# Kernel optimization log

Measured on AMD Instinct MI355X. Metric: run time of the kernel, lower is better.

## Reference

```python
import jax, jax.numpy as jnp
import numpy as np

DIM = 128
HEADS = 4
WIN = 7
N = WIN * WIN  # 49 tokens per window
B = 64         # images
BDIM = 64      # windows per image (56/7)^2
B_ = B * BDIM  # 4096 total windows
HEAD_DIM = DIM // HEADS
SCALE = HEAD_DIM ** (-0.5)


def _rel_index():
    ch, cw = np.meshgrid(np.arange(WIN), np.arange(WIN), indexing='ij')
    coords = np.stack([ch.ravel(), cw.ravel()])            # [2, N]
    rel = coords[:, :, None] - coords[:, None, :]          # [2, N, N]
    rel = rel.transpose(1, 2, 0).astype(np.int32)
    rel[:, :, 0] += WIN - 1
    rel[:, :, 1] += WIN - 1
    rel[:, :, 0] *= 2 * WIN - 1
    return jnp.asarray(rel.sum(-1))                        # [N, N] in [0, 169)


def setup_inputs() -> dict:
    key = jax.random.key(0)
    ks = jax.random.split(key, 7)
    return {
        'x': jax.random.normal(ks[0], (B_, N, DIM), jnp.float32),
        'q_global': jax.random.normal(ks[1], (B, 1, HEADS, N, HEAD_DIM), jnp.float32),
        'rel_bias_table': jax.random.normal(ks[2], (169, HEADS), jnp.float32) * 0.02,
        'W_kv': jax.random.normal(ks[3], (DIM, 2 * DIM), jnp.float32) / np.sqrt(DIM),
        'b_kv': jnp.zeros((2 * DIM,), jnp.float32),
        'W_proj': jax.random.normal(ks[4], (DIM, DIM), jnp.float32) / np.sqrt(DIM),
        'b_proj': jnp.zeros((DIM,), jnp.float32),
        'rel_index': _rel_index(),
    }


def reference(x, q_global, rel_bias_table, W_kv, b_kv, W_proj, b_proj, rel_index):
    Bw, n, C = x.shape
    Bg = q_global.shape[0]
    bdim = Bw // Bg
    # kv projection: [B_, N, 2, H, hd] -> k, v each [B_, H, N, hd]
    kv = (x @ W_kv + b_kv).reshape(Bw, n, 2, HEADS, HEAD_DIM)
    kv = kv.transpose(2, 0, 3, 1, 4)
    k, v = kv[0], kv[1]
    # broadcast global q over windows of each image
    q = jnp.broadcast_to(q_global, (Bg, bdim, HEADS, n, HEAD_DIM)).reshape(Bw, HEADS, n, HEAD_DIM)
    attn = jnp.einsum('bhnd,bhmd->bhnm', q * SCALE, k)
    bias = rel_bias_table[rel_index]                        # [N, N, H]
    attn = attn + bias.transpose(2, 0, 1)[None]
    attn = jax.nn.softmax(attn, axis=-1)
    out = jnp.einsum('bhnm,bhmd->bhnd', attn, v)
    out = out.transpose(0, 2, 1, 3).reshape(Bw, n, C)
    return out @ W_proj + b_proj
```

## Files before the change

### kernel.cpp

```cpp
#include <hip/hip_runtime.h>

#define SCALE 0.17677669529663687f

typedef __attribute__((ext_vector_type(8))) short bf16x8;
typedef __attribute__((ext_vector_type(4))) float f32x4;

__device__ inline short cvt_bf16(float f) {
    union { float f; unsigned u; } v; v.f = f;
    unsigned r = v.u + 0x7fffu + ((v.u >> 16) & 1u);
    return (short)(r >> 16);
}
__device__ inline short cvt_bf16_fast(float f) {
    union { float f; unsigned u; } v; v.f = f;
    return (short)((v.u + 0x8000u) >> 16);
}
__device__ inline unsigned pack_bf16x2(float f0, float f1) {
    union { float f; unsigned u; } a, b; a.f = f0; b.f = f1;
    return __builtin_amdgcn_perm(b.u + 0x8000u, a.u + 0x8000u, 0x07060302u);
}

#define WS_WPT  32768
#define WS_QW   49152
#define WS_BIAS 450560

__global__ void prep_kernel(const float* __restrict__ qg,
                            const float* __restrict__ rbt,
                            const float* __restrict__ wkv,
                            const float* __restrict__ wpj,
                            const int*   __restrict__ ridx,
                            short* __restrict__ ws) {
    int i = blockIdx.x * 256 + threadIdx.x;
    if (i < 32768) {
        int c = i >> 7, k = i & 127;
        ws[i] = cvt_bf16(wkv[k * 256 + c]);
        return;
    }
    i -= 32768;
    if (i < 16384) {
        int c = i >> 7, k = i & 127;
        ws[WS_WPT + i] = cvt_bf16(wpj[k * 128 + c]);
        return;
    }
    i -= 16384;
    if (i < 100352) {
        float4 q4 = *(const float4*)(qg + (long)i * 4);
        unsigned lo = (unsigned)(unsigned short)cvt_bf16(q4.x * SCALE) |
                      ((unsigned)(unsigned short)cvt_bf16(q4.y * SCALE) << 16);
        unsigned hi = (unsigned)(unsigned short)cvt_bf16(q4.z * SCALE) |
                      ((unsigned)(unsigned short)cvt_bf16(q4.w * SCALE) << 16);
        uint2 u; u.x = lo; u.y = hi;
        *(uint2*)(ws + WS_QW + (long)i * 4) = u;
        return;
    }
    i -= 100352;
    if (i < 12544) {
        int h = i / 3136, rem = i % 3136, ir = rem >> 6, j = rem & 63;
        float* bias = (float*)(ws + WS_BIAS);
        bias[i] = (j < 49) ? rbt[ridx[ir * 49 + j] * 4 + h] : 0.f;
    }
}

#define PSLOT   3136
#define VOFF    12544
#define VSTR    56
#define SMEM_SZ 19776

__global__ __launch_bounds__(256, 4) void win_attn_kernel(
        const float* __restrict__ x,
        const short* __restrict__ ws,
        const float* __restrict__ bkv,
        const float* __restrict__ bpj,
        float* __restrict__ out) {
    const int b    = blockIdx.x;
    const int img  = b >> 6;
    const int tid  = threadIdx.x;
    const int w    = tid >> 6;
    const int lane = tid & 63;
    const int quad = lane >> 4;
    const int l16  = lane & 15;

    const short* wkvt  = ws;
    const short* wpt   = ws + WS_WPT;
    const short* qw    = ws + WS_QW;
    const float* biasb = (const float*)(ws + WS_BIAS);

    __shared__ __align__(16) short smem[SMEM_SZ];
    short* xs = smem;
    short* os = smem;

    if (tid < 64) smem[19712 + tid] = 0;

    const f32x4 fzero = {0.f, 0.f, 0.f, 0.f};
    const int h = w;

    const float* xb = x + (long)b * 49 * 128;
    #pragma unroll
    for (int it = 0; it < 4; ++it) {
        int chunk = tid + it * 256;
        if (chunk < 784) {
            int row = chunk >> 4, c8 = (chunk & 15) * 8;
            const float* p = xb + row * 128 + c8;
            float4 a = *(const float4*)p;
            float4 c = *(const float4*)(p + 4);
            union { uint4 u; bf16x8 v; } pk;
            pk.u.x = pack_bf16x2(a.x, a.y);
            pk.u.y = pack_bf16x2(a.z, a.w);
            pk.u.z = pack_bf16x2(c.x, c.y);
            pk.u.w = pack_bf16x2(c.z, c.w);
            *(bf16x8*)(xs + row * 136 + c8) = pk.v;
        }
    }
    __syncthreads();

    f32x4 acc[4][4];
    #pragma unroll
    for (int nt = 0; nt < 4; ++nt)
        #pragma unroll
        for (int mi = 0; mi < 4; ++mi) acc[nt][mi] = fzero;

    #pragma unroll
    for (int kk = 0; kk < 4; ++kk) {
        bf16x8 bfr[4];
        #pragma unroll
        for (int nt = 0; nt < 4; ++nt)
            bfr[nt] = *(const bf16x8*)(wkvt + ((w * 4 + nt) * 16 + l16) * 128 + kk * 32 + quad * 8);
        #pragma unroll
        for (int mi = 0; mi < 4; ++mi) {
            int tok = mi * 16 + l16; if (tok > 48) tok = 48;
            bf16x8 af = *(const bf16x8*)(xs + tok * 136 + kk * 32 + quad * 8);
            #pragma unroll
            for (int nt = 0; nt < 4; ++nt)
                acc[nt][mi] = __builtin_amdgcn_mfma_f32_16x16x32_bf16(af, bfr[nt], acc[nt][mi], 0, 0, 0);
        }
    }
    __syncthreads();

    #pragma unroll
    for (int nt = 0; nt < 4; ++nt) {
        const int c = (w * 4 + nt) * 16 + l16;
        const float bv = bkv[c];
        if (c < 128) {
            int hh = c >> 5, d = c & 31;
            short* kdst = smem + hh * PSLOT + d;
            #pragma unroll
            for (int mi = 0; mi < 4; ++mi)
                #pragma unroll
                for (int r = 0; r < 4; ++r) {
                    int tok = mi * 16 + quad * 4 + r;
                    kdst[tok * 40] = cvt_bf16_fast(acc[nt][mi][r] + bv);
                }
        } else {
            int cv = c - 128, hh = cv >> 5, d = cv & 31;
            short* vdst = smem + VOFF + (hh * 32 + d) * VSTR;
            #pragma unroll
            for (int mi = 0; mi < 4; ++mi) {
                int tok0 = mi * 16 + quad * 4;
                if (tok0 < VSTR) {
                    *(unsigned*)(vdst + tok0)     = pack_bf16x2(acc[nt][mi][0] + bv, acc[nt][mi][1] + bv);
                    *(unsigned*)(vdst + tok0 + 2) = pack_bf16x2(acc[nt][mi][2] + bv, acc[nt][mi][3] + bv);
                }
            }
        }
    }
    __syncthreads();

    short* ksh = smem + h * PSLOT;
    const short* qh = qw + (long)(img * 4 + h) * 49 * 32;
    bf16x8 qfrag[4];
    #pragma unroll
    for (int ni = 0; ni < 4; ++ni) {
        int i = ni * 16 + l16; if (i > 48) i = 48;
        qfrag[ni] = *(const bf16x8*)(qh + i * 32 + quad * 8);
    }
    bf16x8 kfrag[4];
    #pragma unroll
    for (int mi = 0; mi < 4; ++mi)
        kfrag[mi] = *(const bf16x8*)(ksh + (mi * 16 + l16) * 40 + quad * 8);

    #pragma unroll
    for (int ni = 0; ni < 4; ++ni) {
        f32x4 sacc[4] = {fzero, fzero, fzero, fzero};
        #pragma unroll
        for (int mi = 0; mi < 4; ++mi)
            sacc[mi] = __builtin_amdgcn_mfma_f32_16x16x32_bf16(kfrag[mi], qfrag[ni], sacc[mi], 0, 0, 0);

        int itok = ni * 16 + l16;
        int ic = itok > 48 ? 48 : itok;
        const float* bp = biasb + (h * 49 + ic) * 64;
        float v[16];
        #pragma unroll
        for (int mi = 0; mi < 4; ++mi) {
            float4 b4 = *(const float4*)(bp + mi * 16 + quad * 4);
            float bb[4] = {b4.x, b4.y, b4.z, b4.w};
            #pragma unroll
            for (int r = 0; r < 4; ++r) {
                int j = mi * 16 + quad * 4 + r;
                v[mi * 4 + r] = (j < 49) ? (sacc[mi][r] + bb[r]) : -3.0e38f;
            }
        }
        float m = v[0];
        #pragma unroll
        for (int t = 1; t < 16; ++t) m = fmaxf(m, v[t]);
        m = fmaxf(m, __shfl_xor(m, 16, 64));
        m = fmaxf(m, __shfl_xor(m, 32, 64));
        float sum = 0.f;
        #pragma unroll
        for (int t = 0; t < 16; ++t) { float e = __expf(v[t] - m); v[t] = e; sum += e; }
        sum += __shfl_xor(sum, 16, 64);
        sum += __shfl_xor(sum, 32, 64);
        float inv = 1.0f / sum;
        if (itok < 49) {
            #pragma unroll
            for (int mi = 0; mi < 4; ++mi) {
                int jo8 = mi * 2 + (quad >> 1);
                int off = itok * 64 + ((jo8 ^ (itok & 7)) << 3) + ((quad & 1) << 2);
                uint2 u;
                u.x = pack_bf16x2(v[mi * 4 + 0] * inv, v[mi * 4 + 1] * inv);
                u.y = pack_bf16x2(v[mi * 4 + 2] * inv, v[mi * 4 + 3] * inv);
                *(uint2*)(ksh + off) = u;
            }
        }
    }

    f32x4 oacc[4][2];
    #pragma unroll
    for (int mo = 0; mo < 4; ++mo)
        #pragma unroll
        for (int nt = 0; nt < 2; ++nt) oacc[mo][nt] = fzero;
    #pragma unroll
    for (int kk = 0; kk < 2; ++kk) {
        bf16x8 pfrag[4];
        #pragma unroll
        for (int mo = 0; mo < 4; ++mo) {
            int row = mo * 16 + l16; if (row > 48) row = 48;
            int jo8 = kk * 4 + quad;
            pfrag[mo] = *(const bf16x8*)(ksh + row * 64 + ((jo8 ^ (row & 7)) << 3));
        }
        #pragma unroll
        for (int nt = 0; nt < 2; ++nt) {
            bf16x8 vfrag = *(const bf16x8*)(smem + VOFF + (h * 32 + nt * 16 + l16) * VSTR + kk * 32 + quad * 8);
            #pragma unroll
            for (int mo = 0; mo < 4; ++mo)
                oacc[mo][nt] = __builtin_amdgcn_mfma_f32_16x16x32_bf16(pfrag[mo], vfrag, oacc[mo][nt], 0, 0, 0);
        }
    }
    __syncthreads();

    #pragma unroll
    for (int mo = 0; mo < 4; ++mo)
        #pragma unroll
        for (int nt = 0; nt < 2; ++nt)
            #pragma unroll
            for (int r = 0; r < 4; ++r) {
                int tok = mo * 16 + quad * 4 + r;
                os[tok * 136 + h * 32 + nt * 16 + l16] = cvt_bf16_fast(oacc[mo][nt][r]);
            }
    __syncthreads();

    f32x4 pacc[2][4];
    #pragma unroll
    for (int ct = 0; ct < 2; ++ct)
        #pragma unroll
        for (int mi = 0; mi < 4; ++mi) pacc[ct][mi] = fzero;
    #pragma unroll
    for (int kk = 0; kk < 4; ++kk) {
        bf16x8 ofrag[4];
        #pragma unroll
        for (int mi = 0; mi < 4; ++mi)
            ofrag[mi] = *(const bf16x8*)(os + (mi * 16 + l16) * 136 + kk * 32 + quad * 8);
        #pragma unroll
        for (int ct = 0; ct < 2; ++ct) {
            const int c0 = (w * 2 + ct) * 16;
            bf16x8 wfrag = *(const bf16x8*)(wpt + (c0 + l16) * 128 + kk * 32 + quad * 8);
            #pragma unroll
            for (int mi = 0; mi < 4; ++mi)
                pacc[ct][mi] = __builtin_amdgcn_mfma_f32_16x16x32_bf16(ofrag[mi], wfrag, pacc[ct][mi], 0, 0, 0);
        }
    }
    #pragma unroll
    for (int ct = 0; ct < 2; ++ct) {
        const int c0 = (w * 2 + ct) * 16;
        const float bb = bpj[c0 + l16];
        #pragma unroll
        for (int mi = 0; mi < 4; ++mi)
            #pragma unroll
            for (int r = 0; r < 4; ++r) {
                int tok = mi * 16 + quad * 4 + r;
                if (tok < 49)
                    out[((long)b * 49 + tok) * 128 + c0 + l16] = pacc[ct][mi][r] + bb;
            }
    }
}

extern "C" void kernel_launch(void* const* d_in, const int* in_sizes, int n_in,
                              void* d_out, int out_size, void* d_ws, size_t ws_size,
                              hipStream_t stream) {
    const float* x    = (const float*)d_in[0];
    const float* qg   = (const float*)d_in[1];
    const float* rbt  = (const float*)d_in[2];
    const float* wkv  = (const float*)d_in[3];
    const float* bkv  = (const float*)d_in[4];
    const float* wpj  = (const float*)d_in[5];
    const float* bpj  = (const float*)d_in[6];
    const int*   ridx = (const int*)d_in[7];
    short* ws = (short*)d_ws;

    const int prep_total = 32768 + 16384 + 100352 + 12544;
    prep_kernel<<<(prep_total + 255) / 256, 256, 0, stream>>>(qg, rbt, wkv, wpj, ridx, ws);
    win_attn_kernel<<<4096, 256, 0, stream>>>(x, ws, bkv, bpj, (float*)d_out);
}
```

Measured before the change: 251.8 us.

## Keep V and softmax probabilities in registers, feeding PV MFMA directly per head

Each wave now computes the K and V columns for its own head in the KV projection, so V stays in registers as 16x16x16 MFMA B fragments instead of going through shared memory. The softmax output is packed straight into A fragments for a 16x16x16 bf16 MFMA, removing the P round trip through LDS and two block barriers. LDS use shrinks, allowing launch bounds of 5 blocks per CU, at the cost of more live registers and a smaller-K MFMA instruction for the PV product.

```diff
diff --git a/kernel.cpp b/kernel.cpp
--- a/kernel.cpp
+++ b/kernel.cpp
@@ -3,6 +3,7 @@
 #define SCALE 0.17677669529663687f
 
 typedef __attribute__((ext_vector_type(8))) short bf16x8;
+typedef __attribute__((ext_vector_type(4))) short bf16x4;
 typedef __attribute__((ext_vector_type(4))) float f32x4;
 
 __device__ inline short cvt_bf16(float f) {
@@ -18,6 +19,17 @@
     union { float f; unsigned u; } a, b; a.f = f0; b.f = f1;
     return __builtin_amdgcn_perm(b.u + 0x8000u, a.u + 0x8000u, 0x07060302u);
 }
+
+#if __has_builtin(__builtin_amdgcn_mfma_f32_16x16x16bf16_1k)
+__device__ inline f32x4 mfma16x16(bf16x4 a, bf16x4 b, f32x4 c) {
+    return __builtin_amdgcn_mfma_f32_16x16x16bf16_1k(a, b, c, 0, 0, 0);
+}
+#else
+__device__ inline f32x4 mfma16x16(bf16x4 a, bf16x4 b, f32x4 c) {
+    asm("v_mfma_f32_16x16x16_bf16 %0, %1, %2, %0" : "+v"(c) : "v"(a), "v"(b));
+    return c;
+}
+#endif
 
 #define WS_WPT  32768
 #define WS_QW   49152
@@ -60,12 +72,11 @@
     }
 }
 
-#define PSLOT   3136
-#define VOFF    12544
-#define VSTR    56
-#define SMEM_SZ 19776
-
-__global__ __launch_bounds__(256, 4) void win_attn_kernel(
+#define KOFF    6664
+#define KSLOT   1960
+#define SMEM_SZ 14504
+
+__global__ __launch_bounds__(256, 5) void win_attn_kernel(
         const float* __restrict__ x,
         const short* __restrict__ ws,
         const float* __restrict__ bkv,
@@ -87,8 +98,6 @@
     __shared__ __align__(16) short smem[SMEM_SZ];
     short* xs = smem;
     short* os = smem;
-
-    if (tid < 64) smem[19712 + tid] = 0;
 
     const f32x4 fzero = {0.f, 0.f, 0.f, 0.f};
     const int h = w;
@@ -122,8 +131,10 @@
     for (int kk = 0; kk < 4; ++kk) {
         bf16x8 bfr[4];
         #pragma unroll
-        for (int nt = 0; nt < 4; ++nt)
-            bfr[nt] = *(const bf16x8*)(wkvt + ((w * 4 + nt) * 16 + l16) * 128 + kk * 32 + quad * 8);
+        for (int nt = 0; nt < 4; ++nt) {
+            int col = ((nt < 2) ? (h * 32 + nt * 16) : (128 + h * 32 + (nt - 2) * 16)) + l16;
+            bfr[nt] = *(const bf16x8*)(wkvt + col * 128 + kk * 32 + quad * 8);
+        }
         #pragma unroll
         for (int mi = 0; mi < 4; ++mi) {
             int tok = mi * 16 + l16; if (tok > 48) tok = 48;
@@ -133,61 +144,53 @@
                 acc[nt][mi] = __builtin_amdgcn_mfma_f32_16x16x32_bf16(af, bfr[nt], acc[nt][mi], 0, 0, 0);
         }
     }
-    __syncthreads();
-
-    #pragma unroll
-    for (int nt = 0; nt < 4; ++nt) {
-        const int c = (w * 4 + nt) * 16 + l16;
-        const float bv = bkv[c];
-        if (c < 128) {
-            int hh = c >> 5, d = c & 31;
-            short* kdst = smem + hh * PSLOT + d;
-            #pragma unroll
-            for (int mi = 0; mi < 4; ++mi)
-                #pragma unroll
-                for (int r = 0; r < 4; ++r) {
-                    int tok = mi * 16 + quad * 4 + r;
-                    kdst[tok * 40] = cvt_bf16_fast(acc[nt][mi][r] + bv);
-                }
-        } else {
-            int cv = c - 128, hh = cv >> 5, d = cv & 31;
-            short* vdst = smem + VOFF + (hh * 32 + d) * VSTR;
-            #pragma unroll
-            for (int mi = 0; mi < 4; ++mi) {
-                int tok0 = mi * 16 + quad * 4;
-                if (tok0 < VSTR) {
-                    *(unsigned*)(vdst + tok0)     = pack_bf16x2(acc[nt][mi][0] + bv, acc[nt][mi][1] + bv);
-                    *(unsigned*)(vdst + tok0 + 2) = pack_bf16x2(acc[nt][mi][2] + bv, acc[nt][mi][3] + bv);
-                }
-            }
-        }
-    }
-    __syncthreads();
-
-    short* ksh = smem + h * PSLOT;
+
+    short* ksl = smem + KOFF + h * KSLOT;
+    #pragma unroll
+    for (int nt = 0; nt < 2; ++nt) {
+        const int d = nt * 16 + l16;
+        const float bv = bkv[h * 32 + d];
+        short* kdst = ksl + d;
+        #pragma unroll
+        for (int mi = 0; mi < 4; ++mi)
+            #pragma unroll
+            for (int r = 0; r < 4; ++r) {
+                int tok = mi * 16 + quad * 4 + r;
+                if (tok < 49) kdst[tok * 40] = cvt_bf16_fast(acc[nt][mi][r] + bv);
+            }
+    }
+    bf16x4 vfrag[2][4];
+    #pragma unroll
+    for (int nv = 0; nv < 2; ++nv) {
+        const float bv = bkv[128 + h * 32 + nv * 16 + l16];
+        #pragma unroll
+        for (int kt = 0; kt < 4; ++kt) {
+            union { unsigned u[2]; bf16x4 v; } pk;
+            pk.u[0] = pack_bf16x2(acc[nv + 2][kt][0] + bv, acc[nv + 2][kt][1] + bv);
+            pk.u[1] = pack_bf16x2(acc[nv + 2][kt][2] + bv, acc[nv + 2][kt][3] + bv);
+            vfrag[nv][kt] = pk.v;
+        }
+    }
+
     const short* qh = qw + (long)(img * 4 + h) * 49 * 32;
-    bf16x8 qfrag[4];
+    f32x4 oacc[4][2];
+    #pragma unroll
+    for (int mo = 0; mo < 4; ++mo)
+        #pragma unroll
+        for (int nv = 0; nv < 2; ++nv) oacc[mo][nv] = fzero;
+
     #pragma unroll
     for (int ni = 0; ni < 4; ++ni) {
-        int i = ni * 16 + l16; if (i > 48) i = 48;
-        qfrag[ni] = *(const bf16x8*)(qh + i * 32 + quad * 8);
-    }
-    bf16x8 kfrag[4];
-    #pragma unroll
-    for (int mi = 0; mi < 4; ++mi)
-        kfrag[mi] = *(const bf16x8*)(ksh + (mi * 16 + l16) * 40 + quad * 8);
-
-    #pragma unroll
-    for (int ni = 0; ni < 4; ++ni) {
+        int ic = ni * 16 + l16; if (ic > 48) ic = 48;
+        bf16x8 qf = *(const bf16x8*)(qh + ic * 32 + quad * 8);
         f32x4 sacc[4] = {fzero, fzero, fzero, fzero};
         #pragma unroll
-        for (int mi = 0; mi < 4; ++mi)
-            sacc[mi] = __builtin_amdgcn_mfma_f32_16x16x32_bf16(kfrag[mi], qfrag[ni], sacc[mi], 0, 0, 0);
-
-        int itok = ni * 16 + l16;
-        int ic = itok > 48 ? 48 : itok;
+        for (int mi = 0; mi < 4; ++mi) {
+            int kr = mi * 16 + l16; if (kr > 48) kr = 48;
+            bf16x8 kf = *(const bf16x8*)(ksl + kr * 40 + quad * 8);
+            sacc[mi] = __builtin_amdgcn_mfma_f32_16x16x32_bf16(kf, qf, sacc[mi], 0, 0, 0);
+        }
         const float* bp = biasb + (h * 49 + ic) * 64;
-        float v[16];
         #pragma unroll
         for (int mi = 0; mi < 4; ++mi) {
             float4 b4 = *(const float4*)(bp + mi * 16 + quad * 4);
@@ -195,65 +198,48 @@
             #pragma unroll
             for (int r = 0; r < 4; ++r) {
                 int j = mi * 16 + quad * 4 + r;
-                v[mi * 4 + r] = (j < 49) ? (sacc[mi][r] + bb[r]) : -3.0e38f;
-            }
-        }
-        float m = v[0];
-        #pragma unroll
-        for (int t = 1; t < 16; ++t) m = fmaxf(m, v[t]);
+                sacc[mi][r] = (j < 49) ? (sacc[mi][r] + bb[r]) : -3.0e38f;
+            }
+        }
+        float m = -3.0e38f;
+        #pragma unroll
+        for (int mi = 0; mi < 4; ++mi)
+            #pragma unroll
+            for (int r = 0; r < 4; ++r) m = fmaxf(m, sacc[mi][r]);
         m = fmaxf(m, __shfl_xor(m, 16, 64));
         m = fmaxf(m, __shfl_xor(m, 32, 64));
         float sum = 0.f;
         #pragma unroll
-        for (int t = 0; t < 16; ++t) { float e = __expf(v[t] - m); v[t] = e; sum += e; }
+        for (int mi = 0; mi < 4; ++mi)
+            #pragma unroll
+            for (int r = 0; r < 4; ++r) {
+                float e = __expf(sacc[mi][r] - m);
+                sacc[mi][r] = e; sum += e;
+            }
         sum += __shfl_xor(sum, 16, 64);
         sum += __shfl_xor(sum, 32, 64);
         float inv = 1.0f / sum;
-        if (itok < 49) {
-            #pragma unroll
-            for (int mi = 0; mi < 4; ++mi) {
-                int jo8 = mi * 2 + (quad >> 1);
-                int off = itok * 64 + ((jo8 ^ (itok & 7)) << 3) + ((quad & 1) << 2);
-                uint2 u;
-                u.x = pack_bf16x2(v[mi * 4 + 0] * inv, v[mi * 4 + 1] * inv);
-                u.y = pack_bf16x2(v[mi * 4 + 2] * inv, v[mi * 4 + 3] * inv);
-                *(uint2*)(ksh + off) = u;
-            }
-        }
-    }
-
-    f32x4 oacc[4][2];
+        #pragma unroll
+        for (int kt = 0; kt < 4; ++kt) {
+            union { unsigned u[2]; bf16x4 v; } pk;
+            pk.u[0] = pack_bf16x2(sacc[kt][0] * inv, sacc[kt][1] * inv);
+            pk.u[1] = pack_bf16x2(sacc[kt][2] * inv, sacc[kt][3] * inv);
+            #pragma unroll
+            for (int nv = 0; nv < 2; ++nv)
+                oacc[ni][nv] = mfma16x16(pk.v, vfrag[nv][kt], oacc[ni][nv]);
+        }
+    }
+
+    __syncthreads();
+
     #pragma unroll
     for (int mo = 0; mo < 4; ++mo)
         #pragma unroll
-        for (int nt = 0; nt < 2; ++nt) oacc[mo][nt] = fzero;
-    #pragma unroll
-    for (int kk = 0; kk < 2; ++kk) {
-        bf16x8 pfrag[4];
-        #pragma unroll
-        for (int mo = 0; mo < 4; ++mo) {
-            int row = mo * 16 + l16; if (row > 48) row = 48;
-            int jo8 = kk * 4 + quad;
-            pfrag[mo] = *(const bf16x8*)(ksh + row * 64 + ((jo8 ^ (row & 7)) << 3));
-        }
-        #pragma unroll
-        for (int nt = 0; nt < 2; ++nt) {
-            bf16x8 vfrag = *(const bf16x8*)(smem + VOFF + (h * 32 + nt * 16 + l16) * VSTR + kk * 32 + quad * 8);
-            #pragma unroll
-            for (int mo = 0; mo < 4; ++mo)
-                oacc[mo][nt] = __builtin_amdgcn_mfma_f32_16x16x32_bf16(pfrag[mo], vfrag, oacc[mo][nt], 0, 0, 0);
-        }
-    }
-    __syncthreads();
-
-    #pragma unroll
-    for (int mo = 0; mo < 4; ++mo)
-        #pragma unroll
-        for (int nt = 0; nt < 2; ++nt)
+        for (int nv = 0; nv < 2; ++nv)
             #pragma unroll
             for (int r = 0; r < 4; ++r) {
                 int tok = mo * 16 + quad * 4 + r;
-                os[tok * 136 + h * 32 + nt * 16 + l16] = cvt_bf16_fast(oacc[mo][nt][r]);
+                os[tok * 136 + h * 32 + nv * 16 + l16] = cvt_bf16_fast(oacc[mo][nv][r]);
             }
     __syncthreads();
 
```

Result: slower. 319.6 us (+26.9%).
